# Optimization experiments

Hardware: AMD Instinct MI355X
Metric: run time of the kernel (lower is better)

The kernel has to match this reference:

```python
import jax, jax.numpy as jnp
import numpy as np

N, L, H, D = 4, 8192, 8, 64  # batch, seq len, heads, per-head dim
DIM = H * D


def _log_exp_kernel(x):
    # log(1 + exp(x)) positive feature map (softplus)
    return jax.nn.softplus(x)


def setup_inputs() -> dict:
    key = jax.random.key(0)
    k0, k1, k2, k3, k4 = jax.random.split(key, 5)
    s = 1.0 / np.sqrt(DIM).astype(np.float32)
    return {
        "query": jax.random.normal(k0, (N, L, DIM), jnp.float32),
        "key": jax.random.normal(k1, (N, L, DIM), jnp.float32),
        "Wq": jax.random.normal(k2, (DIM, DIM), jnp.float32) * s,
        "Wk": jax.random.normal(k3, (DIM, DIM), jnp.float32) * s,
        "Wv": jax.random.normal(k4, (DIM, DIM), jnp.float32) * s,
    }


def _causal_linear_attention(q, k, v):
    # q, k: (N,H,L,D) kernelized features; v: (N,H,L,D)
    # out[t] = (q_t . S_t) / (q_t . z_t), S_t = sum_{s<=t} k_s v_s^T, z_t = sum_{s<=t} k_s
    qs = jnp.moveaxis(q, 2, 0)  # (L,N,H,D)
    ks = jnp.moveaxis(k, 2, 0)
    vs = jnp.moveaxis(v, 2, 0)
    S0 = jnp.zeros((q.shape[0], q.shape[1], q.shape[3], v.shape[3]), q.dtype)
    z0 = jnp.zeros((q.shape[0], q.shape[1], q.shape[3]), q.dtype)

    def step(carry, xs):
        S, z = carry
        qt, kt, vt = xs  # each (N,H,D)
        S = S + kt[..., :, None] * vt[..., None, :]  # (N,H,D,D)
        z = z + kt
        num = jnp.einsum('nhd,nhde->nhe', qt, S)
        den = jnp.einsum('nhd,nhd->nh', qt, z)
        return (S, z), num / den[..., None]

    _, out = jax.lax.scan(step, (S0, z0), (qs, ks, vs))  # out: (L,N,H,D)
    return jnp.moveaxis(out, 0, 2)  # (N,H,L,D)


def reference(query, key, Wq, Wk, Wv):
    n, Lq, dim = query.shape
    # projections (torch Linear, no bias: x @ W.T), kernel applied in forward...
    q = _log_exp_kernel(query @ Wq.T).reshape(n, Lq, H, D).transpose(0, 2, 1, 3)
    k = _log_exp_kernel(key @ Wk.T).reshape(n, Lq, H, D).transpose(0, 2, 1, 3)
    v = (key @ Wv.T).reshape(n, Lq, H, D).transpose(0, 2, 1, 3)
    # ...and again inside _attention_linear (faithful to the source)
    q = _log_exp_kernel(q)
    k = _log_exp_kernel(k)
    att = _causal_linear_attention(q, k, v)  # (N,H,L,D)
    return att.transpose(0, 2, 1, 3).reshape(n, Lq, H * D)
```

## Files before the change

### kernel.cpp

```cpp
#include <hip/hip_runtime.h>


using bf16x8 = __attribute__((ext_vector_type(8))) short;
using u16x8  = __attribute__((ext_vector_type(8))) unsigned short;
using f32x4  = __attribute__((ext_vector_type(4))) float;

#define L_SEQ   8192
#define NCHUNK  128
#define RECB    8448

__device__ __forceinline__ float bf2f(unsigned short u) {
  union { unsigned int i; float f; } c; c.i = ((unsigned int)u) << 16; return c.f;
}
__device__ __forceinline__ unsigned short f2bf(float f) {
  union { float f; unsigned int i; } c; c.f = f;
  unsigned int r = c.i + 0x7fffu + ((c.i >> 16) & 1u);
  return (unsigned short)(r >> 16);
}
__device__ __forceinline__ float sp_(float x) {
  return (x > 20.0f) ? x : __logf(1.0f + __expf(x));
}
__device__ __forceinline__ void gll16(const void* g, void* l) {
  __builtin_amdgcn_global_load_lds(
      (const __attribute__((address_space(1))) unsigned int*)g,
      (__attribute__((address_space(3))) unsigned int*)l, 16, 0, 0);
}

__global__ void cvt_all(const float* __restrict__ q, const float* __restrict__ k,
                        const float* __restrict__ wq, const float* __restrict__ wk,
                        const float* __restrict__ wv,
                        unsigned short* __restrict__ qo, unsigned short* __restrict__ ko,
                        unsigned short* __restrict__ wqo, unsigned short* __restrict__ wko,
                        unsigned short* __restrict__ wvo) {
  const int stride = gridDim.x * blockDim.x;
  for (int i = blockIdx.x * blockDim.x + threadIdx.x; i < 8585216; i += stride) {
    const float* src; unsigned short* dst; int off;
    if (i < 4194304)      { src = q;  dst = qo;  off = i; }
    else if (i < 8388608) { src = k;  dst = ko;  off = i - 4194304; }
    else if (i < 8454144) { src = wq; dst = wqo; off = i - 8388608; }
    else if (i < 8519680) { src = wk; dst = wko; off = i - 8454144; }
    else                  { src = wv; dst = wvo; off = i - 8519680; }
    float4 v = ((const float4*)src)[off];
    ushort4 o;
    o.x = f2bf(v.x); o.y = f2bf(v.y); o.z = f2bf(v.z); o.w = f2bf(v.w);
    ((ushort4*)dst)[off] = o;
  }
}

template <int MODE>
__global__ __launch_bounds__(256, 2) void gemm_proj(const unsigned short* __restrict__ A,
                                                    const unsigned short* __restrict__ W,
                                                    unsigned short* __restrict__ out) {
  __shared__ char As[16384];
  __shared__ char Bs[16384];
  const int tid  = threadIdx.x;
  const int lane = tid & 63;
  const int wave = tid >> 6;
  const int l15  = lane & 15;
  const int lg   = lane >> 4;
  const int wr   = (wave >> 1) * 64;
  const int wc   = (wave & 1) * 64;
  const int bm   = blockIdx.x * 128;
  const int bn   = blockIdx.y * 128;
  const char* Abytes = (const char*)A;
  const char* Wbytes = (const char*)W;

  f32x4 acc[4][4] = {};

  for (int ks = 0; ks < 8; ++ks) {
#pragma unroll
    for (int it = 0; it < 4; ++it) {
      const int p  = wave * 4096 + it * 1024 + lane * 16;
      const int r  = p >> 7;
      const int cb = (p & 127) ^ ((r & 7) << 4);
      gll16(Abytes + (size_t)(bm + r) * 1024 + ks * 128 + cb, As + wave * 4096 + it * 1024);
      gll16(Wbytes + (size_t)(bn + r) * 1024 + ks * 128 + cb, Bs + wave * 4096 + it * 1024);
    }
    __syncthreads();
#pragma unroll
    for (int kk = 0; kk < 2; ++kk) {
      const int cb = kk * 64 + lg * 16;
      bf16x8 af[4], bw[4];
#pragma unroll
      for (int mi = 0; mi < 4; ++mi) {
        const int r = wr + mi * 16 + l15;
        af[mi] = *(const bf16x8*)(As + r * 128 + (cb ^ ((r & 7) << 4)));
      }
#pragma unroll
      for (int ni = 0; ni < 4; ++ni) {
        const int r = wc + ni * 16 + l15;
        bw[ni] = *(const bf16x8*)(Bs + r * 128 + (cb ^ ((r & 7) << 4)));
      }
#pragma unroll
      for (int mi = 0; mi < 4; ++mi)
#pragma unroll
        for (int ni = 0; ni < 4; ++ni)
          acc[mi][ni] = __builtin_amdgcn_mfma_f32_16x16x32_bf16(af[mi], bw[ni], acc[mi][ni], 0, 0, 0);
    }
    __syncthreads();
  }

#pragma unroll
  for (int mi = 0; mi < 4; ++mi)
#pragma unroll
    for (int ni = 0; ni < 4; ++ni)
#pragma unroll
      for (int j = 0; j < 4; ++j) {
        const int m = bm + wr + mi * 16 + lg * 4 + j;
        const int n = bn + wc + ni * 16 + l15;
        float x = acc[mi][ni][j];
        const int nb = m >> 13;
        const int l  = m & 8191;
        const int h  = n >> 6;
        if (MODE == 0) {
          x = sp_(sp_(x));
          const int d = n & 63;
          out[(((size_t)(nb * 8 + h) * 8192 + l) << 6) + d] = f2bf(x);
        } else {
          const int e = n & 63;
          const int cc = l >> 6, s = l & 63;
          out[(((size_t)((nb * 8 + h) * 128 + cc) * 64 + e) << 6) + s] = f2bf(x);
        }
      }
}

__global__ __launch_bounds__(256, 4) void chunk_sums(const unsigned short* __restrict__ kb,
                                                     const unsigned short* __restrict__ vt,
                                                     char* __restrict__ S) {
  const int b  = blockIdx.x;
  const int nh = b >> 7, c = b & 127;
  __shared__ char Kt[8192];
  __shared__ char STs[8192];
  const int tid = threadIdx.x, lane = tid & 63, wave = tid >> 6;
  const int l15 = lane & 15, lg = lane >> 4;
  const unsigned short* kch = kb + ((size_t)(nh * L_SEQ + c * 64) << 6);
  const unsigned short* vch = vt + ((size_t)b << 12);

  {
    const int s = tid >> 2, d0 = (tid & 3) << 4;
    u16x8 a = *(const u16x8*)(kch + s * 64 + d0);
    u16x8 bb = *(const u16x8*)(kch + s * 64 + d0 + 8);
#pragma unroll
    for (int i = 0; i < 8; ++i) {
      const int d = d0 + i;
      *(unsigned short*)(Kt + d * 128 + ((2 * s) ^ ((d & 7) << 4))) = a[i];
    }
#pragma unroll
    for (int i = 0; i < 8; ++i) {
      const int d = d0 + 8 + i;
      *(unsigned short*)(Kt + d * 128 + ((2 * s) ^ ((d & 7) << 4))) = bb[i];
    }
  }
  __syncthreads();

  f32x4 acc[4] = {};
#pragma unroll
  for (int kk = 0; kk < 2; ++kk) {
    bf16x8 av = *(const bf16x8*)(vch + (wave * 16 + l15) * 64 + kk * 32 + lg * 8);
#pragma unroll
    for (int ni = 0; ni < 4; ++ni) {
      const int d = ni * 16 + l15;
      bf16x8 bk = *(const bf16x8*)(Kt + d * 128 + ((kk * 64 + lg * 16) ^ ((d & 7) << 4)));
      acc[ni] = __builtin_amdgcn_mfma_f32_16x16x32_bf16(av, bk, acc[ni], 0, 0, 0);
    }
  }

  char* rec = S + (size_t)b * RECB;

  if (tid < 64) {
    float z = 0.f;
#pragma unroll
    for (int kk = 0; kk < 8; ++kk) {
      bf16x8 kv = *(const bf16x8*)(Kt + tid * 128 + ((kk * 16) ^ ((tid & 7) << 4)));
#pragma unroll
      for (int i = 0; i < 8; ++i) z += bf2f(kv[i]);
    }
    *(float*)(rec + 8192 + tid * 4) = z;
  }

#pragma unroll
  for (int ni = 0; ni < 4; ++ni)
#pragma unroll
    for (int j = 0; j < 4; ++j) {
      const int e = wave * 16 + lg * 4 + j, d = ni * 16 + l15;
      *(unsigned short*)(STs + e * 128 + d * 2) = f2bf(acc[ni][j]);
    }
  __syncthreads();
  {
    const int off = tid * 32;
    *(u16x8*)(rec + off)      = *(const u16x8*)(STs + off);
    *(u16x8*)(rec + off + 16) = *(const u16x8*)(STs + off + 16);
  }
}

__global__ void scan_chunks(char* __restrict__ S) {
  const int g = blockIdx.x * 256 + threadIdx.x;
  if (g < 65536) {
    const int nh = g >> 11, pr = g & 2047;
    char* p = S + (size_t)nh * NCHUNK * RECB + pr * 4;
    float a0 = 0.f, a1 = 0.f;
    for (int c = 0; c < NCHUNK; ++c) {
      const unsigned int u = *(unsigned int*)p;
      const float t0 = bf2f((unsigned short)(u & 0xffff));
      const float t1 = bf2f((unsigned short)(u >> 16));
      *(unsigned int*)p = (unsigned int)f2bf(a0) | ((unsigned int)f2bf(a1) << 16);
      a0 += t0; a1 += t1;
      p += RECB;
    }
  } else if (g < 67584) {
    const int idx = g - 65536;
    const int nh = idx >> 6, d = idx & 63;
    char* p = S + (size_t)nh * NCHUNK * RECB + 8192 + d * 4;
    float a = 0.f;
    for (int c = 0; c < NCHUNK; ++c) {
      const float t = *(float*)p; *(float*)p = a; a += t; p += RECB;
    }
  }
}

__global__ __launch_bounds__(256, 2) void attn_out(const unsigned short* __restrict__ qb,
                                                   const unsigned short* __restrict__ kb,
                                                   const unsigned short* __restrict__ vt,
                                                   const char* __restrict__ S,
                                                   float* __restrict__ out) {
  const int b  = blockIdx.x;
  const int nh = b >> 7, c = b & 127;
  const int nb = nh >> 3, h = nh & 7;
  __shared__ char Qs[8192], Ks[8192], Vs[8192], STs[8192], Ps[8192];
  __shared__ float zsh[64], dzh[64];
  const int tid = threadIdx.x, lane = tid & 63, wave = tid >> 6;
  const int l15 = lane & 15, lg = lane >> 4;

  const char* qch = (const char*)(qb + ((size_t)(nh * L_SEQ + c * 64) << 6));
  const char* kch = (const char*)(kb + ((size_t)(nh * L_SEQ + c * 64) << 6));
  const char* vch = (const char*)(vt + ((size_t)b << 12));
  const char* rb  = S + (size_t)b * RECB;

#pragma unroll
  for (int it = 0; it < 2; ++it) {
    const int p  = wave * 2048 + it * 1024 + lane * 16;
    const int r  = p >> 7;
    const int cb = (p & 127) ^ ((r & 7) << 4);
    const int src = r * 128 + cb;
    gll16(qch + src, Qs + wave * 2048 + it * 1024);
    gll16(kch + src, Ks + wave * 2048 + it * 1024);
    gll16(vch + src, Vs + wave * 2048 + it * 1024);
    gll16(rb + src,  STs + wave * 2048 + it * 1024);
  }
  if (tid < 64) zsh[tid] = *(const float*)(rb + 8192 + tid * 4);
  __syncthreads();

  {
    const int t = tid >> 2, p4 = tid & 3;
    float dq = 0.f;
#pragma unroll
    for (int half = 0; half < 2; ++half) {
      const int d0 = p4 * 16 + half * 8;
      const int cb = (d0 * 2) ^ ((t & 7) << 4);
      u16x8 qv = *(const u16x8*)(Qs + t * 128 + cb);
#pragma unroll
      for (int i = 0; i < 8; ++i) dq += bf2f(qv[i]) * zsh[d0 + i];
    }
    dq += __shfl_xor(dq, 1);
    dq += __shfl_xor(dq, 2);
    if (p4 == 0) dzh[t] = dq;
  }
  __syncthreads();

  f32x4 accA[4] = {};
#pragma unroll
  for (int kk = 0; kk < 2; ++kk) {
    const int cb = kk * 64 + lg * 16;
    const int rq = wave * 16 + l15;
    bf16x8 aq = *(const bf16x8*)(Qs + rq * 128 + (cb ^ ((rq & 7) << 4)));
#pragma unroll
    for (int ni = 0; ni < 4; ++ni) {
      const int rk = ni * 16 + l15;
      bf16x8 bk = *(const bf16x8*)(Ks + rk * 128 + (cb ^ ((rk & 7) << 4)));
      accA[ni] = __builtin_amdgcn_mfma_f32_16x16x32_bf16(aq, bk, accA[ni], 0, 0, 0);
    }
  }

  float den4[4];
#pragma unroll
  for (int j = 0; j < 4; ++j) {
    const int t = wave * 16 + lg * 4 + j;
    float rs = 0.f;
#pragma unroll
    for (int ni = 0; ni < 4; ++ni) {
      const int s = ni * 16 + l15;
      const float v = (s <= t) ? accA[ni][j] : 0.f;
      const unsigned short pb = f2bf(v);
      rs += bf2f(pb);
      *(unsigned short*)(Ps + t * 128 + ((s * 2) ^ ((t & 7) << 4))) = pb;
    }
    rs += __shfl_xor(rs, 1);
    rs += __shfl_xor(rs, 2);
    rs += __shfl_xor(rs, 4);
    rs += __shfl_xor(rs, 8);
    den4[j] = rs + dzh[t];
  }
  __syncthreads();

  f32x4 accO[4] = {};
#pragma unroll
  for (int kk = 0; kk < 2; ++kk) {
    const int cb = kk * 64 + lg * 16;
    const int rp = wave * 16 + l15;
    bf16x8 ap = *(const bf16x8*)(Ps + rp * 128 + (cb ^ ((rp & 7) << 4)));
    bf16x8 aq = *(const bf16x8*)(Qs + rp * 128 + (cb ^ ((rp & 7) << 4)));
#pragma unroll
    for (int ni = 0; ni < 4; ++ni) {
      const int rv = ni * 16 + l15;
      bf16x8 bv = *(const bf16x8*)(Vs + rv * 128 + (cb ^ ((rv & 7) << 4)));
      bf16x8 bs = *(const bf16x8*)(STs + rv * 128 + (cb ^ ((rv & 7) << 4)));
      accO[ni] = __builtin_amdgcn_mfma_f32_16x16x32_bf16(ap, bv, accO[ni], 0, 0, 0);
      accO[ni] = __builtin_amdgcn_mfma_f32_16x16x32_bf16(aq, bs, accO[ni], 0, 0, 0);
    }
  }

#pragma unroll
  for (int ni = 0; ni < 4; ++ni) {
    const int e = ni * 16 + l15;
#pragma unroll
    for (int j = 0; j < 4; ++j) {
      const int t = wave * 16 + lg * 4 + j;
      out[((size_t)(nb * L_SEQ + c * 64 + t) << 9) + h * 64 + e] = accO[ni][j] / den4[j];
    }
  }
}

extern "C" void kernel_launch(void* const* d_in, const int* in_sizes, int n_in,
                              void* d_out, int out_size, void* d_ws, size_t ws_size,
                              hipStream_t stream) {
  (void)in_sizes; (void)n_in; (void)out_size; (void)ws_size;
  const float* query = (const float*)d_in[0];
  const float* key   = (const float*)d_in[1];
  const float* Wq    = (const float*)d_in[2];
  const float* Wk    = (const float*)d_in[3];
  const float* Wv    = (const float*)d_in[4];
  float* out = (float*)d_out;
  char* ws = (char*)d_ws;

  unsigned short* qb  = (unsigned short*)(ws);
  unsigned short* kb  = (unsigned short*)(ws + 33554432);
  unsigned short* vt  = (unsigned short*)(ws + 67108864);
  unsigned short* qbf = (unsigned short*)(ws + 100663296);
  unsigned short* kbf = (unsigned short*)(ws + 134217728);
  char*           Ssum = ws + 100663296;
  unsigned short* wqb = (unsigned short*)(ws + 168820736);
  unsigned short* wkb = (unsigned short*)(ws + 169345024);
  unsigned short* wvb = (unsigned short*)(ws + 169869312);

  cvt_all<<<dim3(2048), dim3(256), 0, stream>>>(query, key, Wq, Wk, Wv, qbf, kbf, wqb, wkb, wvb);

  dim3 gg(256, 4);
  gemm_proj<0><<<gg, dim3(256), 0, stream>>>(qbf, wqb, qb);
  gemm_proj<0><<<gg, dim3(256), 0, stream>>>(kbf, wkb, kb);
  gemm_proj<1><<<gg, dim3(256), 0, stream>>>(kbf, wvb, vt);

  chunk_sums<<<dim3(4096), dim3(256), 0, stream>>>(kb, vt, Ssum);
  scan_chunks<<<dim3(264), dim3(256), 0, stream>>>(Ssum);
  attn_out<<<dim3(4096), dim3(256), 0, stream>>>(qb, kb, vt, Ssum, out);
}
```

Before: 203.7 us.

## Merge three projection GEMMs into one launch with double-buffered LDS staging

Replaces the three separate templated projection GEMM launches with a single kernel whose grid y-dimension selects the Q, K or V projection, so one launch covers all three. The main loop now double-buffers its shared-memory tiles (64KB LDS), issuing the next k-step's async global-to-LDS loads before computing on the current step. The intent is to cut launch overhead and tail effects and to overlap memory loads with MFMA work. The larger LDS footprint may lower occupancy, and the output mode becomes a runtime branch instead of a template parameter.

Result: slower. 235.5 us (+15.6%).

```diff
diff --git a/kernel.cpp b/kernel.cpp
--- a/kernel.cpp
+++ b/kernel.cpp
@@ -47,12 +47,23 @@
   }
 }
 
-template <int MODE>
-__global__ __launch_bounds__(256, 2) void gemm_proj(const unsigned short* __restrict__ A,
-                                                    const unsigned short* __restrict__ W,
-                                                    unsigned short* __restrict__ out) {
-  __shared__ char As[16384];
-  __shared__ char Bs[16384];
+__global__ __launch_bounds__(256, 2) void gemm_all(const unsigned short* __restrict__ qbf,
+                                                   const unsigned short* __restrict__ kbf,
+                                                   const unsigned short* __restrict__ wqb,
+                                                   const unsigned short* __restrict__ wkb,
+                                                   const unsigned short* __restrict__ wvb,
+                                                   unsigned short* __restrict__ qb,
+                                                   unsigned short* __restrict__ kb,
+                                                   unsigned short* __restrict__ vt) {
+  __shared__ char Lds[65536];
+  const int y = blockIdx.y;
+  const unsigned short* A; const unsigned short* W; unsigned short* outp; int mode;
+  if (y < 4)      { A = qbf; W = wqb; outp = qb; mode = 0; }
+  else if (y < 8) { A = kbf; W = wkb; outp = kb; mode = 0; }
+  else            { A = kbf; W = wvb; outp = vt; mode = 1; }
+  const int bn = (y & 3) * 128;
+  const int bm = blockIdx.x * 128;
+
   const int tid  = threadIdx.x;
   const int lane = tid & 63;
   const int wave = tid >> 6;
@@ -60,23 +71,35 @@
   const int lg   = lane >> 4;
   const int wr   = (wave >> 1) * 64;
   const int wc   = (wave & 1) * 64;
-  const int bm   = blockIdx.x * 128;
-  const int bn   = blockIdx.y * 128;
   const char* Abytes = (const char*)A;
   const char* Wbytes = (const char*)W;
 
   f32x4 acc[4][4] = {};
 
+  const int p0 = wave * 4096 + lane * 16;
+
+#define STAGE(buf, ks)                                                                   \
+  {                                                                                      \
+    char* Ab = Lds + (buf) * 32768;                                                      \
+    char* Bb = Ab + 16384;                                                               \
+    _Pragma("unroll")                                                                    \
+    for (int it = 0; it < 4; ++it) {                                                     \
+      const int p  = p0 + it * 1024;                                                     \
+      const int r  = p >> 7;                                                             \
+      const int cb = (p & 127) ^ ((r & 7) << 4);                                         \
+      gll16(Abytes + (size_t)(bm + r) * 1024 + (ks) * 128 + cb, Ab + wave * 4096 + it * 1024); \
+      gll16(Wbytes + (size_t)(bn + r) * 1024 + (ks) * 128 + cb, Bb + wave * 4096 + it * 1024); \
+    }                                                                                    \
+  }
+
+  STAGE(0, 0);
+  __syncthreads();
+
   for (int ks = 0; ks < 8; ++ks) {
-#pragma unroll
-    for (int it = 0; it < 4; ++it) {
-      const int p  = wave * 4096 + it * 1024 + lane * 16;
-      const int r  = p >> 7;
-      const int cb = (p & 127) ^ ((r & 7) << 4);
-      gll16(Abytes + (size_t)(bm + r) * 1024 + ks * 128 + cb, As + wave * 4096 + it * 1024);
-      gll16(Wbytes + (size_t)(bn + r) * 1024 + ks * 128 + cb, Bs + wave * 4096 + it * 1024);
-    }
-    __syncthreads();
+    const int cur = ks & 1;
+    if (ks < 7) STAGE(cur ^ 1, ks + 1);
+    const char* Ab = Lds + cur * 32768;
+    const char* Bb = Ab + 16384;
 #pragma unroll
     for (int kk = 0; kk < 2; ++kk) {
       const int cb = kk * 64 + lg * 16;
@@ -84,12 +107,12 @@
 #pragma unroll
       for (int mi = 0; mi < 4; ++mi) {
         const int r = wr + mi * 16 + l15;
-        af[mi] = *(const bf16x8*)(As + r * 128 + (cb ^ ((r & 7) << 4)));
+        af[mi] = *(const bf16x8*)(Ab + r * 128 + (cb ^ ((r & 7) << 4)));
       }
 #pragma unroll
       for (int ni = 0; ni < 4; ++ni) {
         const int r = wc + ni * 16 + l15;
-        bw[ni] = *(const bf16x8*)(Bs + r * 128 + (cb ^ ((r & 7) << 4)));
+        bw[ni] = *(const bf16x8*)(Bb + r * 128 + (cb ^ ((r & 7) << 4)));
       }
 #pragma unroll
       for (int mi = 0; mi < 4; ++mi)
@@ -99,6 +122,7 @@
     }
     __syncthreads();
   }
+#undef STAGE
 
 #pragma unroll
   for (int mi = 0; mi < 4; ++mi)
@@ -112,14 +136,14 @@
         const int nb = m >> 13;
         const int l  = m & 8191;
         const int h  = n >> 6;
-        if (MODE == 0) {
+        if (mode == 0) {
           x = sp_(sp_(x));
           const int d = n & 63;
-          out[(((size_t)(nb * 8 + h) * 8192 + l) << 6) + d] = f2bf(x);
+          outp[(((size_t)(nb * 8 + h) * 8192 + l) << 6) + d] = f2bf(x);
         } else {
           const int e = n & 63;
           const int cc = l >> 6, s = l & 63;
-          out[(((size_t)((nb * 8 + h) * 128 + cc) * 64 + e) << 6) + s] = f2bf(x);
+          outp[(((size_t)((nb * 8 + h) * 128 + cc) * 64 + e) << 6) + s] = f2bf(x);
         }
       }
 }
@@ -354,10 +378,7 @@
 
   cvt_all<<<dim3(2048), dim3(256), 0, stream>>>(query, key, Wq, Wk, Wv, qbf, kbf, wqb, wkb, wvb);
 
-  dim3 gg(256, 4);
-  gemm_proj<0><<<gg, dim3(256), 0, stream>>>(qbf, wqb, qb);
-  gemm_proj<0><<<gg, dim3(256), 0, stream>>>(kbf, wkb, kb);
-  gemm_proj<1><<<gg, dim3(256), 0, stream>>>(kbf, wvb, vt);
+  gemm_all<<<dim3(256, 12), dim3(256), 0, stream>>>(qbf, kbf, wqb, wkb, wvb, qb, kb, vt);
 
   chunk_sums<<<dim3(4096), dim3(256), 0, stream>>>(kb, vt, Ssum);
   scan_chunks<<<dim3(264), dim3(256), 0, stream>>>(Ssum);
```
